# Kernel tuning notes

Hardware: AMD Instinct MI355X
Metric: run time of the kernel (lower is better)

## Reference

```python
import jax, jax.numpy as jnp
import numpy as np

HID = 1024
VOCAB = 32000


def setup_inputs() -> dict:
    key = jax.random.key(0)
    ks = jax.random.split(key, 10)
    B, T, S, H, V = 64, 128, 128, HID, VOCAB
    s = 1.0 / np.sqrt(H)
    inp = {
        "tgt": jax.random.randint(ks[0], (B, T), 0, V),
        "h0": jax.random.normal(ks[1], (1, B, H), dtype=jnp.float32),
        "c0": jax.random.normal(ks[2], (1, B, H), dtype=jnp.float32),
        "encoder_outputs": jax.random.normal(ks[3], (B, S, H), dtype=jnp.float32),
        "src_lengths": jax.random.randint(ks[4], (B,), 1, S + 1),
        "emb_table": jax.random.normal(ks[5], (V, H), dtype=jnp.float32),
        "w_ih": jax.random.uniform(ks[6], (4 * H, H), minval=-s, maxval=s, dtype=jnp.float32),
        "w_hh": jax.random.uniform(ks[7], (4 * H, H), minval=-s, maxval=s, dtype=jnp.float32),
        "b_ih": jax.random.uniform(ks[8], (4 * H,), minval=-s, maxval=s, dtype=jnp.float32),
        "b_hh": jax.random.uniform(ks[9], (4 * H,), minval=-s, maxval=s, dtype=jnp.float32),
    }
    return inp


def _lstm_scan(xs, h0, c0, w_ih, w_hh, b_ih, b_hh):
    # xs: [T', B, H]; PyTorch gate order i, f, g, o
    def step(carry, x):
        h, c = carry
        gates = x @ w_ih.T + b_ih + h @ w_hh.T + b_hh  # [B, 4H]
        i, f, g, o = jnp.split(gates, 4, axis=-1)
        c = jax.nn.sigmoid(f) * c + jax.nn.sigmoid(i) * jnp.tanh(g)
        h = jax.nn.sigmoid(o) * jnp.tanh(c)
        return (h, c), h

    (h, c), ys = jax.lax.scan(step, (h0, c0), xs)
    return ys, h, c


def reference(tgt, h0, c0, encoder_outputs, src_lengths, emb_table, w_ih, w_hh, b_ih, b_hh):
    # padding_idx=0: that embedding row is pinned to zero
    emb_table = emb_table.at[0].set(0.0)
    embedded = emb_table[tgt]  # [B, T, H]; dropout(p=0) = identity
    T = tgt.shape[1]
    n_steps = T - 1 if T > 1 else 1  # torch loop feeds inputs 0..T-2
    xs = jnp.transpose(embedded[:, :n_steps, :], (1, 0, 2))  # [T', B, H]
    ys, h, c = _lstm_scan(xs, h0[0], c0[0], w_ih, w_hh, b_ih, b_hh)
    outputs = jnp.transpose(ys, (1, 0, 2))  # [B, T', H]; attn=None, dropout=identity
    return outputs, h[None], c[None]
```

## Files before the change

kernel.cpp:

```cpp
#include <hip/hip_runtime.h>
#include <cstdint>
#include <cstddef>

#define HID   1024
#define G4    4096
#define BB    64
#define TSEQ  128
#define NSTEP 127
#define AGT   __HIP_MEMORY_SCOPE_AGENT

typedef __attribute__((ext_vector_type(4))) float f32x4;
typedef __attribute__((ext_vector_type(8))) short bf16x8;

__device__ __forceinline__ unsigned short f2bf(float x) {
  union { float f; unsigned u; } v; v.f = x;
  unsigned r = v.u + 0x7FFF + ((v.u >> 16) & 1);
  return (unsigned short)(r >> 16);
}

__global__ __launch_bounds__(256) void conv_f32_bf16(
    const float* __restrict__ in, unsigned short* __restrict__ out, int n)
{
  int i = (blockIdx.x * 256 + threadIdx.x) * 8;
  if (i >= n) return;
  float4 v0 = *reinterpret_cast<const float4*>(&in[i]);
  float4 v1 = *reinterpret_cast<const float4*>(&in[i + 4]);
  unsigned short u[8];
  u[0] = f2bf(v0.x); u[1] = f2bf(v0.y); u[2] = f2bf(v0.z); u[3] = f2bf(v0.w);
  u[4] = f2bf(v1.x); u[5] = f2bf(v1.y); u[6] = f2bf(v1.z); u[7] = f2bf(v1.w);
  *reinterpret_cast<bf16x8*>(&out[i]) = *reinterpret_cast<bf16x8*>(u);
}

__global__ __launch_bounds__(256) void bias_add(
    const float* __restrict__ b_ih, const float* __restrict__ b_hh,
    float* __restrict__ bias)
{
  int i = blockIdx.x * 256 + threadIdx.x;
  if (i < G4) bias[i] = b_ih[i] + b_hh[i];
}

__global__ __launch_bounds__(256) void conv_A(
    const int* __restrict__ tgt, const float* __restrict__ emb,
    unsigned short* __restrict__ A, int t0, int tc)
{
  int i = blockIdx.x * 256 + threadIdx.x;
  int m  = i >> 7;
  int k8 = (i & 127) * 8;
  int tl = m >> 6, b = m & 63;
  float4 v0 = make_float4(0.f, 0.f, 0.f, 0.f), v1 = v0;
  if (tl < tc) {
    int tok = tgt[b * TSEQ + t0 + tl];
    if (tok != 0) {
      const float* src = &emb[(size_t)tok * HID + k8];
      v0 = *reinterpret_cast<const float4*>(src);
      v1 = *reinterpret_cast<const float4*>(src + 4);
    }
  }
  unsigned short u[8];
  u[0] = f2bf(v0.x); u[1] = f2bf(v0.y); u[2] = f2bf(v0.z); u[3] = f2bf(v0.w);
  u[4] = f2bf(v1.x); u[5] = f2bf(v1.y); u[6] = f2bf(v1.z); u[7] = f2bf(v1.w);
  *reinterpret_cast<bf16x8*>(&A[(size_t)m * HID + k8]) = *reinterpret_cast<bf16x8*>(u);
}

__global__ __launch_bounds__(256) void gin_mfma(
    const unsigned short* __restrict__ A, const unsigned short* __restrict__ W,
    const float* __restrict__ bias, float* __restrict__ gin, int Mvalid)
{
  __shared__ unsigned short As[128 * 40];
  __shared__ unsigned short Bs[128 * 40];

  const int tid = threadIdx.x;
  const int m0 = blockIdx.x * 128, n0 = blockIdx.y * 128;
  const int l  = tid & 63, w = tid >> 6;
  const int wr = w >> 1, wc = w & 1;
  const int lr = l & 15, lh = l >> 4;

  f32x4 acc[4][4];
#pragma unroll
  for (int i = 0; i < 4; ++i)
#pragma unroll
    for (int j = 0; j < 4; ++j) acc[i][j] = (f32x4)0.f;

  for (int kc = 0; kc < HID; kc += 32) {
#pragma unroll
    for (int it = 0; it < 2; ++it) {
      int c = tid + it * 256;
      int row = c >> 2, k8 = (c & 3) * 8;
      *reinterpret_cast<bf16x8*>(&As[row * 40 + k8]) =
          *reinterpret_cast<const bf16x8*>(&A[(size_t)(m0 + row) * HID + kc + k8]);
      *reinterpret_cast<bf16x8*>(&Bs[row * 40 + k8]) =
          *reinterpret_cast<const bf16x8*>(&W[(size_t)(n0 + row) * HID + kc + k8]);
    }
    __syncthreads();

    bf16x8 af[4], bfr[4];
#pragma unroll
    for (int i = 0; i < 4; ++i) {
      af[i]  = *reinterpret_cast<const bf16x8*>(&As[(wr * 64 + i * 16 + lr) * 40 + lh * 8]);
      bfr[i] = *reinterpret_cast<const bf16x8*>(&Bs[(wc * 64 + i * 16 + lr) * 40 + lh * 8]);
    }
#pragma unroll
    for (int i = 0; i < 4; ++i)
#pragma unroll
      for (int j = 0; j < 4; ++j)
        acc[i][j] = __builtin_amdgcn_mfma_f32_16x16x32_bf16(af[i], bfr[j], acc[i][j], 0, 0, 0);
    __syncthreads();
  }

#pragma unroll
  for (int j = 0; j < 4; ++j) {
    int n = n0 + wc * 64 + j * 16 + lr;
    float bn = bias[n];
#pragma unroll
    for (int i = 0; i < 4; ++i) {
      int mb = m0 + wr * 64 + i * 16 + lh * 4;
#pragma unroll
      for (int r = 0; r < 4; ++r) {
        int m = mb + r;
        if (m < Mvalid) gin[(size_t)m * G4 + n] = acc[i][j][r] + bn;
      }
    }
  }
}

__global__ __launch_bounds__(256, 1) void lstm_persist(
    const unsigned short* __restrict__ whh, const float* __restrict__ gin,
    unsigned int* __restrict__ hb0, unsigned int* __restrict__ hb1,
    float* __restrict__ c_ws, const float* __restrict__ c0,
    float* __restrict__ out, unsigned int* __restrict__ flags,
    int t0, int tc)
{
  __shared__ float red[4][4][16][16];

  const int tid = threadIdx.x;
  const int l = tid & 63, w = tid >> 6;
  const int lr = l & 15, lh = l >> 4;
  const int grp = blockIdx.x >> 6;
  const int ub  = blockIdx.x & 63;
  const int b0 = grp * 16;
  const int u0 = ub * 16;

  bf16x8 bw[4][8];
#pragma unroll
  for (int g = 0; g < 4; ++g)
#pragma unroll
    for (int kk = 0; kk < 8; ++kk)
      bw[g][kk] = *reinterpret_cast<const bf16x8*>(
          &whh[(size_t)(g * HID + u0 + lr) * HID + w * 256 + kk * 32 + lh * 8]);

  const int bi = tid >> 4, ui = tid & 15;
  const size_t ci = (size_t)(b0 + bi) * HID + u0 + ui;
  float c_reg = (t0 == 0) ? c0[ci] : c_ws[ci];

  for (int tl = 0; tl < tc; ++tl) {
    const int t = t0 + tl;
    const unsigned int* hin  = (t & 1) ? hb1 : hb0;
    unsigned int*       hout = (t & 1) ? hb0 : hb1;

#pragma unroll
    for (int g = 0; g < 4; ++g)
#pragma unroll
      for (int kk = 0; kk < 8; ++kk)
        asm volatile("" : "+v"(bw[g][kk]));

    float gi[4];
#pragma unroll
    for (int g = 0; g < 4; ++g)
      gi[g] = gin[((size_t)tl * BB + b0 + bi) * G4 + g * HID + u0 + ui];

    if (t > 0) {
      const unsigned int* fl = flags + (((size_t)(t - 1) * 4 + grp) * 64 + l) * 4;
      while (true) {
        unsigned v = __hip_atomic_load(fl, __ATOMIC_RELAXED, AGT);
        if (__all(v != 0)) break;
        __builtin_amdgcn_s_sleep(2);
      }
    }

    bf16x8 af[8];
#pragma unroll
    for (int kk = 0; kk < 8; ++kk) {
      size_t base = ((size_t)(b0 + lr) * HID + (size_t)w * 256 + kk * 32 + lh * 8) >> 1;
      unsigned long long lo = __hip_atomic_load(
          reinterpret_cast<const unsigned long long*>(&hin[base]), __ATOMIC_RELAXED, AGT);
      unsigned long long hi = __hip_atomic_load(
          reinterpret_cast<const unsigned long long*>(&hin[base + 2]), __ATOMIC_RELAXED, AGT);
      union { unsigned long long q[2]; bf16x8 v; } u;
      u.q[0] = lo; u.q[1] = hi;
      af[kk] = u.v;
    }

    f32x4 acc[4];
#pragma unroll
    for (int g = 0; g < 4; ++g) acc[g] = (f32x4)0.f;
#pragma unroll
    for (int kk = 0; kk < 8; ++kk)
#pragma unroll
      for (int g = 0; g < 4; ++g)
        acc[g] = __builtin_amdgcn_mfma_f32_16x16x32_bf16(af[kk], bw[g][kk], acc[g], 0, 0, 0);

#pragma unroll
    for (int g = 0; g < 4; ++g)
#pragma unroll
      for (int r = 0; r < 4; ++r)
        red[w][g][lh * 4 + r][lr] = acc[g][r];
    __syncthreads();

    float gates[4];
#pragma unroll
    for (int g = 0; g < 4; ++g)
      gates[g] = red[0][g][bi][ui] + red[1][g][bi][ui] +
                 red[2][g][bi][ui] + red[3][g][bi][ui] + gi[g];

    float iv = 1.f / (1.f + expf(-gates[0]));
    float fv = 1.f / (1.f + expf(-gates[1]));
    float gv = tanhf(gates[2]);
    float ov = 1.f / (1.f + expf(-gates[3]));
    c_reg = fv * c_reg + iv * gv;
    float hn = ov * tanhf(c_reg);

    unsigned hv = (unsigned)f2bf(hn);
    unsigned pv = (unsigned)__shfl_xor((int)hv, 1);
    if ((tid & 1) == 0) {
      unsigned word = (hv & 0xffffu) | (pv << 16);
      __hip_atomic_store(&hout[ci >> 1], word, __ATOMIC_RELAXED, AGT);
    }

    out[((size_t)(b0 + bi) * NSTEP + t) * HID + u0 + ui] = hn;
    if (t == NSTEP - 1) {
      size_t tail = (size_t)BB * NSTEP * HID;
      out[tail + ci] = hn;
      out[tail + (size_t)BB * HID + ci] = c_reg;
    }

    __syncthreads();
    if (tid == 0)
      __hip_atomic_store(&flags[(((size_t)t * 4 + grp) * 64 + ub) * 4], 1u,
                         __ATOMIC_RELAXED, AGT);
  }
  c_ws[ci] = c_reg;
}

extern "C" void kernel_launch(void* const* d_in, const int* in_sizes, int n_in,
                              void* d_out, int out_size, void* d_ws, size_t ws_size,
                              hipStream_t stream)
{
  const int*   tgt  = (const int*)d_in[0];
  const float* h0   = (const float*)d_in[1];
  const float* c0   = (const float*)d_in[2];
  const float* emb  = (const float*)d_in[5];
  const float* w_ih = (const float*)d_in[6];
  const float* w_hh = (const float*)d_in[7];
  const float* b_ih = (const float*)d_in[8];
  const float* b_hh = (const float*)d_in[9];
  float* out = (float*)d_out;

  const size_t FLAGS_BYTES = (size_t)NSTEP * 4 * 64 * 16;

  char* p = (char*)d_ws;
  unsigned short* wih_bf = (unsigned short*)p; p += (size_t)G4 * HID * 2;
  unsigned short* whh_bf = (unsigned short*)p; p += (size_t)G4 * HID * 2;
  float*          bias   = (float*)p;          p += (size_t)G4 * 4;
  unsigned int*   hb0    = (unsigned int*)p;   p += (size_t)BB * HID * 2;
  unsigned int*   hb1    = (unsigned int*)p;   p += (size_t)BB * HID * 2;
  float*          c_ws   = (float*)p;          p += (size_t)BB * HID * 4;
  unsigned int*   flags  = (unsigned int*)p;   p += FLAGS_BYTES;

  size_t fixed = (size_t)(p - (char*)d_ws);
  size_t rem = (ws_size > fixed) ? ws_size - fixed : 0;
  int Tc = (int)((rem > 262144 ? rem - 262144 : 0) / 1179648);
  if (Tc > NSTEP) Tc = NSTEP;
  if (Tc < 1) return;

  int MtMax = ((Tc * BB + 127) / 128) * 128;
  unsigned short* A_bf = (unsigned short*)p; p += (size_t)MtMax * HID * 2;
  float*          gin  = (float*)p;

  hipMemsetAsync(flags, 0, FLAGS_BYTES, stream);
  conv_f32_bf16<<<dim3((G4 * HID) / 8 / 256), 256, 0, stream>>>(w_ih, wih_bf, G4 * HID);
  conv_f32_bf16<<<dim3((G4 * HID) / 8 / 256), 256, 0, stream>>>(w_hh, whh_bf, G4 * HID);
  bias_add<<<dim3(G4 / 256), 256, 0, stream>>>(b_ih, b_hh, bias);
  conv_f32_bf16<<<dim3((BB * HID) / 8 / 256), 256, 0, stream>>>(h0, (unsigned short*)hb0, BB * HID);

  for (int t0 = 0; t0 < NSTEP; t0 += Tc) {
    int tc = (NSTEP - t0 < Tc) ? (NSTEP - t0) : Tc;
    int Mt = ((tc * BB + 127) / 128) * 128;
    conv_A<<<dim3(Mt / 2), 256, 0, stream>>>(tgt, emb, A_bf, t0, tc);
    gin_mfma<<<dim3(Mt / 128, G4 / 128), 256, 0, stream>>>(A_bf, wih_bf, bias, gin, tc * BB);

    void* kargs[] = { (void*)&whh_bf, (void*)&gin, (void*)&hb0, (void*)&hb1,
                      (void*)&c_ws, (void*)&c0, (void*)&out, (void*)&flags,
                      (void*)&t0, (void*)&tc };
    hipLaunchCooperativeKernel((void*)lstm_persist, dim3(256), dim3(256),
                               kargs, 0, stream);
  }
}
```

Before: 609.5 us.

## Stage recurrent weights in LDS, signal flags earlier, use fast gate math

Moves the per-block W_hh slice out of registers into LDS (64 KB) and reads it back per MFMA, which frees registers. The step-completion flag is now published right after the h store (with an explicit vmcnt wait), before the output writes, so the dependent blocks can start sooner. The spin sleep is shortened, and sigmoid/tanh now use __expf-based approximations. The cost is extra LDS traffic on every step and slightly lower precision in the activations.

```diff
diff --git a/kernel.cpp b/kernel.cpp
--- a/kernel.cpp
+++ b/kernel.cpp
@@ -17,6 +17,8 @@
   unsigned r = v.u + 0x7FFF + ((v.u >> 16) & 1);
   return (unsigned short)(r >> 16);
 }
+__device__ __forceinline__ float fsigm(float x) { return 1.0f / (1.0f + __expf(-x)); }
+__device__ __forceinline__ float ftanh(float x) { return 2.0f / (1.0f + __expf(-2.0f * x)) - 1.0f; }
 
 __global__ __launch_bounds__(256) void conv_f32_bf16(
     const float* __restrict__ in, unsigned short* __restrict__ out, int n)
@@ -130,6 +132,7 @@
     float* __restrict__ out, unsigned int* __restrict__ flags,
     int t0, int tc)
 {
+  __shared__ unsigned short wh_lds[4 * 4 * 8 * 512];
   __shared__ float red[4][4][16][16];
 
   const int tid = threadIdx.x;
@@ -140,28 +143,25 @@
   const int b0 = grp * 16;
   const int u0 = ub * 16;
 
-  bf16x8 bw[4][8];
-#pragma unroll
-  for (int g = 0; g < 4; ++g)
-#pragma unroll
-    for (int kk = 0; kk < 8; ++kk)
-      bw[g][kk] = *reinterpret_cast<const bf16x8*>(
-          &whh[(size_t)(g * HID + u0 + lr) * HID + w * 256 + kk * 32 + lh * 8]);
+  for (int idx = tid; idx < 8192; idx += 256) {
+    int ll = idx & 63, kk = (idx >> 6) & 7, g = (idx >> 9) & 3, ww = (idx >> 11) & 3;
+    bf16x8 v = *reinterpret_cast<const bf16x8*>(
+        &whh[(size_t)(g * HID + u0 + (ll & 15)) * HID + ww * 256 + kk * 32 + (ll >> 4) * 8]);
+    *reinterpret_cast<bf16x8*>(&wh_lds[(size_t)idx * 8]) = v;
+  }
 
   const int bi = tid >> 4, ui = tid & 15;
   const size_t ci = (size_t)(b0 + bi) * HID + u0 + ui;
   float c_reg = (t0 == 0) ? c0[ci] : c_ws[ci];
+
+  __syncthreads();
+
+  const size_t hbase = ((size_t)(b0 + lr) * HID) >> 1;
 
   for (int tl = 0; tl < tc; ++tl) {
     const int t = t0 + tl;
     const unsigned int* hin  = (t & 1) ? hb1 : hb0;
     unsigned int*       hout = (t & 1) ? hb0 : hb1;
-
-#pragma unroll
-    for (int g = 0; g < 4; ++g)
-#pragma unroll
-      for (int kk = 0; kk < 8; ++kk)
-        asm volatile("" : "+v"(bw[g][kk]));
 
     float gi[4];
 #pragma unroll
@@ -173,31 +173,30 @@
       while (true) {
         unsigned v = __hip_atomic_load(fl, __ATOMIC_RELAXED, AGT);
         if (__all(v != 0)) break;
-        __builtin_amdgcn_s_sleep(2);
+        __builtin_amdgcn_s_sleep(1);
       }
     }
 
-    bf16x8 af[8];
+    f32x4 acc[4];
+#pragma unroll
+    for (int g = 0; g < 4; ++g) acc[g] = (f32x4)0.f;
 #pragma unroll
     for (int kk = 0; kk < 8; ++kk) {
-      size_t base = ((size_t)(b0 + lr) * HID + (size_t)w * 256 + kk * 32 + lh * 8) >> 1;
+      size_t base = hbase + (size_t)w * 128 + kk * 16 + lh * 4;
       unsigned long long lo = __hip_atomic_load(
           reinterpret_cast<const unsigned long long*>(&hin[base]), __ATOMIC_RELAXED, AGT);
       unsigned long long hi = __hip_atomic_load(
           reinterpret_cast<const unsigned long long*>(&hin[base + 2]), __ATOMIC_RELAXED, AGT);
       union { unsigned long long q[2]; bf16x8 v; } u;
       u.q[0] = lo; u.q[1] = hi;
-      af[kk] = u.v;
-    }
-
-    f32x4 acc[4];
-#pragma unroll
-    for (int g = 0; g < 4; ++g) acc[g] = (f32x4)0.f;
-#pragma unroll
-    for (int kk = 0; kk < 8; ++kk)
-#pragma unroll
-      for (int g = 0; g < 4; ++g)
-        acc[g] = __builtin_amdgcn_mfma_f32_16x16x32_bf16(af[kk], bw[g][kk], acc[g], 0, 0, 0);
+      bf16x8 af = u.v;
+#pragma unroll
+      for (int g = 0; g < 4; ++g) {
+        bf16x8 bw = *reinterpret_cast<const bf16x8*>(
+            &wh_lds[(size_t)(((w * 4 + g) * 8 + kk) * 512 + l * 8)]);
+        acc[g] = __builtin_amdgcn_mfma_f32_16x16x32_bf16(af, bw, acc[g], 0, 0, 0);
+      }
+    }
 
 #pragma unroll
     for (int g = 0; g < 4; ++g)
@@ -212,12 +211,12 @@
       gates[g] = red[0][g][bi][ui] + red[1][g][bi][ui] +
                  red[2][g][bi][ui] + red[3][g][bi][ui] + gi[g];
 
-    float iv = 1.f / (1.f + expf(-gates[0]));
-    float fv = 1.f / (1.f + expf(-gates[1]));
-    float gv = tanhf(gates[2]);
-    float ov = 1.f / (1.f + expf(-gates[3]));
+    float iv = fsigm(gates[0]);
+    float fv = fsigm(gates[1]);
+    float gv = ftanh(gates[2]);
+    float ov = fsigm(gates[3]);
     c_reg = fv * c_reg + iv * gv;
-    float hn = ov * tanhf(c_reg);
+    float hn = ov * ftanh(c_reg);
 
     unsigned hv = (unsigned)f2bf(hn);
     unsigned pv = (unsigned)__shfl_xor((int)hv, 1);
@@ -225,6 +224,11 @@
       unsigned word = (hv & 0xffffu) | (pv << 16);
       __hip_atomic_store(&hout[ci >> 1], word, __ATOMIC_RELAXED, AGT);
     }
+    asm volatile("s_waitcnt vmcnt(0)");
+    __syncthreads();
+    if (tid == 0)
+      __hip_atomic_store(&flags[(((size_t)t * 4 + grp) * 64 + ub) * 4], 1u,
+                         __ATOMIC_RELAXED, AGT);
 
     out[((size_t)(b0 + bi) * NSTEP + t) * HID + u0 + ui] = hn;
     if (t == NSTEP - 1) {
@@ -232,11 +236,6 @@
       out[tail + ci] = hn;
       out[tail + (size_t)BB * HID + ci] = c_reg;
     }
-
-    __syncthreads();
-    if (tid == 0)
-      __hip_atomic_store(&flags[(((size_t)t * 4 + grp) * 64 + ub) * 4], 1u,
-                         __ATOMIC_RELAXED, AGT);
   }
   c_ws[ci] = c_reg;
 }
@@ -258,13 +257,13 @@
   const size_t FLAGS_BYTES = (size_t)NSTEP * 4 * 64 * 16;
 
   char* p = (char*)d_ws;
-  unsigned short* wih_bf = (unsigned short*)p; p += (size_t)G4 * HID * 2;
-  unsigned short* whh_bf = (unsigned short*)p; p += (size_t)G4 * HID * 2;
-  float*          bias   = (float*)p;          p += (size_t)G4 * 4;
-  unsigned int*   hb0    = (unsigned int*)p;   p += (size_t)BB * HID * 2;
-  unsigned int*   hb1    = (unsigned int*)p;   p += (size_t)BB * HID * 2;
-  float*          c_ws   = (float*)p;          p += (size_t)BB * HID * 4;
-  unsigned int*   flags  = (unsigned int*)p;   p += FLAGS_BYTES;
+  unsigned short* wih_bf = (unsigned short*)p;  p += (size_t)G4 * HID * 2;
+  unsigned short* whh_bf = (unsigned short*)p;  p += (size_t)G4 * HID * 2;
+  float*          bias   = (float*)p;           p += (size_t)G4 * 4;
+  unsigned int*   hb0    = (unsigned int*)p;    p += (size_t)BB * HID * 2;
+  unsigned int*   hb1    = (unsigned int*)p;    p += (size_t)BB * HID * 2;
+  float*          c_ws   = (float*)p;           p += (size_t)BB * HID * 4;
+  unsigned int*   flags  = (unsigned int*)p;    p += FLAGS_BYTES;
 
   size_t fixed = (size_t)(p - (char*)d_ws);
   size_t rem = (ws_size > fixed) ? ws_size - fixed : 0;
```

New measurement: 829.5 us. 36.1% more time.
